# Kernel tuning notes

Hardware: AMD Instinct MI355X
Metric: run time of the kernel (lower is better)

Reference implementation:

```python
import jax, jax.numpy as jnp
import numpy as np

N_NODES = 100000
N_EDGES = 1600000
N_GRAPHS = 64
F = 128  # feature_dim == hidden_dim == embedding_dim
NUM_CONVS = 3


def _layernorm(h, g, b, eps=1e-5):
    mu = jnp.mean(h, axis=-1, keepdims=True)
    var = jnp.var(h, axis=-1, keepdims=True)
    return (h - mu) * jax.lax.rsqrt(var + eps) * g + b


def setup_inputs() -> dict:
    key = jax.random.key(0)
    ks = jax.random.split(key, 12)
    s = 1.0 / np.sqrt(F)
    return {
        "x": jax.random.normal(ks[0], (N_NODES, F), jnp.float32),
        "edge_index": jax.random.randint(ks[1], (2, N_EDGES), 0, N_NODES, jnp.int32),
        "batch_vec": jnp.sort(jax.random.randint(ks[2], (N_NODES,), 0, N_GRAPHS, jnp.int32)),
        "gammas": 1.0 + 0.1 * jax.random.normal(ks[3], (N_GRAPHS, NUM_CONVS), jnp.float32),
        "betas": 0.1 * jax.random.normal(ks[4], (N_GRAPHS, NUM_CONVS), jnp.float32),
        "pre_W0": s * jax.random.normal(ks[5], (F, F), jnp.float32),
        "pre_b0": jnp.zeros((F,), jnp.float32),
        "pre_W1": s * jax.random.normal(ks[6], (F, F), jnp.float32),
        "pre_b1": jnp.zeros((F,), jnp.float32),
        "gin_W": s * jax.random.normal(ks[7], (NUM_CONVS, 2, F, F), jnp.float32),
        "gin_b": jnp.zeros((NUM_CONVS, 2, F), jnp.float32),
        "post_W0": (1.0 / np.sqrt(5 * F)) * jax.random.normal(ks[8], (5 * F, F), jnp.float32),
        "post_b0": jnp.zeros((F,), jnp.float32),
        "post_ln_g": jnp.ones((F,), jnp.float32),
        "post_ln_b": jnp.zeros((F,), jnp.float32),
        "post_W1": s * jax.random.normal(ks[9], (F, F), jnp.float32),
        "post_b1": jnp.zeros((F,), jnp.float32),
    }


def reference(x, edge_index, batch_vec, gammas, betas,
              pre_W0, pre_b0, pre_W1, pre_b1,
              gin_W, gin_b,
              post_W0, post_b0, post_ln_g, post_ln_b, post_W1, post_b1):
    n = x.shape[0]
    src, dst = edge_index[0], edge_index[1]

    # preprocess MLP (2 layers, ReLU between, batch_norm='none')
    h = jnp.dot(jax.nn.relu(jnp.dot(x, pre_W0) + pre_b0), pre_W1) + pre_b1
    jump_xs = [x, h]

    # per-node FiLM coefficients (repeat_interleave over sorted batch == gather)
    g_nodes = gammas[batch_vec]  # [N, num_convs]
    b_nodes = betas[batch_vec]   # [N, num_convs]

    for i in range(NUM_CONVS):
        # GINConv, eps=0: MLP(h_i + sum_{j->i} h_j)
        aggr = jax.ops.segment_sum(h[src], dst, num_segments=n)
        z = h + aggr
        h = jnp.dot(jax.nn.relu(jnp.dot(z, gin_W[i, 0]) + gin_b[i, 0]), gin_W[i, 1]) + gin_b[i, 1]
        # FiLM modulation
        h = h * g_nodes[:, i:i + 1] + b_nodes[:, i:i + 1]
        jump_xs.append(h)

    # jumping knowledge 'cat'
    h = jnp.concatenate(jump_xs, axis=-1)  # [N, feature + 4*hidden]

    # postprocess MLP with LayerNorm (batch_norm='layer'); dropout p=0 (eval)
    z = jnp.dot(h, post_W0) + post_b0
    z = jax.nn.relu(_layernorm(z, post_ln_g, post_ln_b))
    return jnp.dot(z, post_W1) + post_b1
```

## Files before the change

kernel.cpp:

```cpp
#include <hip/hip_runtime.h>
#include <stdint.h>

#define FDIM 128
constexpr int EP_NONE = 0, EP_RELU = 1, EP_FILM = 2, EP_LNRELU = 3;

typedef __attribute__((ext_vector_type(8))) short short8v;
typedef __attribute__((ext_vector_type(4))) float f32x4;
typedef __attribute__((ext_vector_type(4))) unsigned int u32x4;

struct Srcs { const float* p[5]; };
struct WPtrs { const float* p[14]; };

__device__ __forceinline__ short f2bf(float f) {
  unsigned u = __float_as_uint(f);
  u = (u + 0x7fffu + ((u >> 16) & 1u)) >> 16;
  return (short)u;
}
__device__ __forceinline__ float bf2f(short s) {
  return __uint_as_float(((unsigned)(unsigned short)s) << 16);
}


__global__ __launch_bounds__(256)
void k_hist(const int* __restrict__ dst, int* __restrict__ cnt, int E) {
  int e = blockIdx.x * 256 + threadIdx.x;
  if (e < E) atomicAdd(&cnt[dst[e]], 1);
}

__global__ __launch_bounds__(1024)
void k_scan_block(const int* __restrict__ cnt, int* __restrict__ scanned,
                  int* __restrict__ partials, int n) {
  __shared__ int sd[1024];
  int tid = threadIdx.x;
  int i = blockIdx.x * 1024 + tid;
  int v = (i < n) ? cnt[i] : 0;
  sd[tid] = v; __syncthreads();
  for (int off = 1; off < 1024; off <<= 1) {
    int t = (tid >= off) ? sd[tid - off] : 0;
    __syncthreads();
    sd[tid] += t;
    __syncthreads();
  }
  if (i < n) scanned[i] = sd[tid] - v;
  if (tid == 1023) partials[blockIdx.x] = sd[1023];
}

__global__ __launch_bounds__(128)
void k_scan_small(const int* __restrict__ partials, int* __restrict__ p2, int nb) {
  __shared__ int sd[128];
  int tid = threadIdx.x;
  int v = (tid < nb) ? partials[tid] : 0;
  sd[tid] = v; __syncthreads();
  for (int off = 1; off < 128; off <<= 1) {
    int t = (tid >= off) ? sd[tid - off] : 0;
    __syncthreads();
    sd[tid] += t;
    __syncthreads();
  }
  p2[tid] = sd[tid] - v;
}

__global__ __launch_bounds__(256)
void k_finalize(const int* __restrict__ scanned, const int* __restrict__ p2,
                int* __restrict__ indptr, int* __restrict__ cursor, int n, int E) {
  int i = blockIdx.x * 256 + threadIdx.x;
  if (i < n) {
    int v = scanned[i] + p2[i >> 10];
    indptr[i] = v;
    cursor[i] = v;
  }
  if (i == 0) indptr[n] = E;
}

__global__ __launch_bounds__(256)
void k_scatter(const int* __restrict__ src, const int* __restrict__ dst,
               int* __restrict__ cursor, int* __restrict__ eids, int E) {
  int e = blockIdx.x * 256 + threadIdx.x;
  if (e < E) {
    int p = atomicAdd(&cursor[dst[e]], 1);
    eids[p] = src[e];
  }
}


__global__ __launch_bounds__(256)
void k_aggr(const float* __restrict__ h, const int* __restrict__ indptr,
            const int* __restrict__ eids, float* __restrict__ z, int n) {
  int lane = threadIdx.x & 63;
  int node = blockIdx.x * 4 + (threadIdx.x >> 6);
  if (node >= n) return;
  float2 acc = *(const float2*)&h[(size_t)node * FDIM + lane * 2];
  int s = indptr[node], e = indptr[node + 1];
  for (int base = s; base < e; base += 64) {
    int cnt = min(64, e - base);
    int eid = (base + lane < e) ? eids[base + lane] : 0;
    int j = 0;
    for (; j + 8 <= cnt; j += 8) {
      float2 v[8];
      #pragma unroll
      for (int t = 0; t < 8; ++t) {
        int sn = __shfl(eid, j + t, 64);
        v[t] = *(const float2*)&h[(size_t)sn * FDIM + lane * 2];
      }
      #pragma unroll
      for (int t = 0; t < 8; ++t) { acc.x += v[t].x; acc.y += v[t].y; }
    }
    for (; j < cnt; ++j) {
      int sn = __shfl(eid, j, 64);
      float2 hv = *(const float2*)&h[(size_t)sn * FDIM + lane * 2];
      acc.x += hv.x; acc.y += hv.y;
    }
  }
  *(float2*)&z[(size_t)node * FDIM + lane * 2] = acc;
}


__global__ __launch_bounds__(256)
void k_wt(WPtrs wp, short* __restrict__ wtHi, short* __restrict__ wtLo) {
  const int m = blockIdx.x;
  const float* __restrict__ W = wp.p[m];
  const int t = threadIdx.x;
  #pragma unroll
  for (int u = 0; u < 8; ++u) {
    int chunk = t + u * 256;
    int c = chunk >> 4, kc = chunk & 15;
    short8v hi, lo;
    #pragma unroll
    for (int j = 0; j < 8; ++j) {
      float w = W[(kc * 8 + j) * FDIM + c];
      short h = f2bf(w);
      hi[j] = h;
      lo[j] = f2bf(w - bf2f(h));
    }
    int off = m * 16384 + c * FDIM + kc * 8;
    *(short8v*)(wtHi + off) = hi;
    *(short8v*)(wtLo + off) = lo;
  }
}


__device__ __forceinline__ void load_panel(float4 (&P)[2][4][2], const float* __restrict__ A,
                                           int row0, int lr, int lg, int n) {
  const float4 f4z = {0.f, 0.f, 0.f, 0.f};
  #pragma unroll
  for (int s = 0; s < 2; ++s) {
    const int r = row0 + s * 16 + lr;
    const bool ok = r < n;
    const float* Ar = A + (size_t)r * FDIM + lg * 8;
    #pragma unroll
    for (int k = 0; k < 4; ++k) {
      P[s][k][0] = ok ? *(const float4*)(Ar + k * 32) : f4z;
      P[s][k][1] = ok ? *(const float4*)(Ar + k * 32 + 4) : f4z;
    }
  }
}

__device__ __forceinline__ void compute_panel(const float4 (&P)[2][4][2], f32x4 (&acc)[2][8],
                                              const short* __restrict__ wtHi,
                                              const short* __restrict__ wtLo,
                                              int wbase, int lr, int lg) {
  #pragma unroll
  for (int k = 0; k < 4; ++k) {
    short8v ah[2], al[2];
    #pragma unroll
    for (int s = 0; s < 2; ++s) {
      const float vv[8] = {P[s][k][0].x, P[s][k][0].y, P[s][k][0].z, P[s][k][0].w,
                           P[s][k][1].x, P[s][k][1].y, P[s][k][1].z, P[s][k][1].w};
      #pragma unroll
      for (int j = 0; j < 8; ++j) {
        short h = f2bf(vv[j]);
        ah[s][j] = h;
        al[s][j] = f2bf(vv[j] - bf2f(h));
      }
    }
    #pragma unroll
    for (int f = 0; f < 8; ++f) {
      const int boff = wbase + (f * 16 + lr) * FDIM + k * 32 + lg * 8;
      short8v bh = *(const short8v*)(wtHi + boff);
      short8v bl = *(const short8v*)(wtLo + boff);
      acc[0][f] = __builtin_amdgcn_mfma_f32_16x16x32_bf16(ah[0], bh, acc[0][f], 0, 0, 0);
      acc[1][f] = __builtin_amdgcn_mfma_f32_16x16x32_bf16(ah[1], bh, acc[1][f], 0, 0, 0);
      acc[0][f] = __builtin_amdgcn_mfma_f32_16x16x32_bf16(al[0], bh, acc[0][f], 0, 0, 0);
      acc[1][f] = __builtin_amdgcn_mfma_f32_16x16x32_bf16(al[1], bh, acc[1][f], 0, 0, 0);
      acc[0][f] = __builtin_amdgcn_mfma_f32_16x16x32_bf16(ah[0], bl, acc[0][f], 0, 0, 0);
      acc[1][f] = __builtin_amdgcn_mfma_f32_16x16x32_bf16(ah[1], bl, acc[1][f], 0, 0, 0);
    }
  }
}

template<int NSRC, int EPI1, int EPI2>
__global__ __launch_bounds__(256, 2)
void k_mlp(Srcs srcs, const short* __restrict__ wtHi, const short* __restrict__ wtLo,
           int m0, int m1, const float* __restrict__ b1, const float* __restrict__ b2,
           float* __restrict__ out, int n,
           const int* __restrict__ bvec, const float* __restrict__ gam,
           const float* __restrict__ bet, int conv,
           const float* __restrict__ lng, const float* __restrict__ lnb) {
  __shared__ unsigned int lds[128 * FDIM];

  const int tid = threadIdx.x;
  const int lane = tid & 63;
  const int w = tid >> 6;
  const int lr = lane & 15;
  const int lg = lane >> 4;
  const int row0 = blockIdx.x * 128 + w * 32;

  f32x4 acc[2][8];
  #pragma unroll
  for (int s = 0; s < 2; ++s)
    #pragma unroll
    for (int f = 0; f < 8; ++f) acc[s][f] = (f32x4){0.f, 0.f, 0.f, 0.f};

  float4 P0[2][4][2], P1[2][4][2];
  load_panel(P0, srcs.p[0], row0, lr, lg, n);
  if constexpr (NSRC >= 2) load_panel(P1, srcs.p[1], row0, lr, lg, n);
  compute_panel(P0, acc, wtHi, wtLo, (m0 + 0) * 16384, lr, lg);
  if constexpr (NSRC >= 3) load_panel(P0, srcs.p[2], row0, lr, lg, n);
  if constexpr (NSRC >= 2) compute_panel(P1, acc, wtHi, wtLo, (m0 + 1) * 16384, lr, lg);
  if constexpr (NSRC >= 4) load_panel(P1, srcs.p[3], row0, lr, lg, n);
  if constexpr (NSRC >= 3) compute_panel(P0, acc, wtHi, wtLo, (m0 + 2) * 16384, lr, lg);
  if constexpr (NSRC >= 5) load_panel(P0, srcs.p[4], row0, lr, lg, n);
  if constexpr (NSRC >= 4) compute_panel(P1, acc, wtHi, wtLo, (m0 + 3) * 16384, lr, lg);
  if constexpr (NSRC >= 5) compute_panel(P0, acc, wtHi, wtLo, (m0 + 4) * 16384, lr, lg);

  {
    float bb[8];
    #pragma unroll
    for (int f = 0; f < 8; ++f) bb[f] = b1[f * 16 + lr];
    #pragma unroll
    for (int s = 0; s < 2; ++s) {
      #pragma unroll
      for (int f = 0; f < 8; ++f)
        #pragma unroll
        for (int i = 0; i < 4; ++i) acc[s][f][i] += bb[f];

      if constexpr (EPI1 == EP_LNRELU) {
        float sm[4] = {0.f, 0.f, 0.f, 0.f}, sq[4] = {0.f, 0.f, 0.f, 0.f};
        #pragma unroll
        for (int f = 0; f < 8; ++f)
          #pragma unroll
          for (int i = 0; i < 4; ++i) {
            float v = acc[s][f][i];
            sm[i] += v; sq[i] += v * v;
          }
        #pragma unroll
        for (int m = 1; m < 16; m <<= 1)
          #pragma unroll
          for (int i = 0; i < 4; ++i) {
            sm[i] += __shfl_xor(sm[i], m, 64);
            sq[i] += __shfl_xor(sq[i], m, 64);
          }
        float gg[8], bn[8];
        #pragma unroll
        for (int f = 0; f < 8; ++f) { gg[f] = lng[f * 16 + lr]; bn[f] = lnb[f * 16 + lr]; }
        #pragma unroll
        for (int i = 0; i < 4; ++i) {
          const float mu = sm[i] * (1.f / FDIM);
          const float var = sq[i] * (1.f / FDIM) - mu * mu;
          const float rs = rsqrtf(var + 1e-5f);
          #pragma unroll
          for (int f = 0; f < 8; ++f)
            acc[s][f][i] = fmaxf((acc[s][f][i] - mu) * rs * gg[f] + bn[f], 0.f);
        }
      } else {
        #pragma unroll
        for (int f = 0; f < 8; ++f)
          #pragma unroll
          for (int i = 0; i < 4; ++i) acc[s][f][i] = fmaxf(acc[s][f][i], 0.f);
      }

      #pragma unroll
      for (int f = 0; f < 8; ++f)
        #pragma unroll
        for (int i = 0; i < 4; ++i) {
          float v = acc[s][f][i];
          short hi = f2bf(v);
          short lo = f2bf(v - bf2f(hi));
          unsigned pk = (unsigned)(unsigned short)hi | ((unsigned)(unsigned short)lo << 16);
          const int rl = w * 32 + s * 16 + 4 * lg + i;
          const int c = f * 16 + lr;
          lds[rl * FDIM + (c ^ ((rl & 7) * 8))] = pk;
        }
    }
  }
  __syncthreads();

  f32x4 acc2[2][8];
  #pragma unroll
  for (int s = 0; s < 2; ++s)
    #pragma unroll
    for (int f = 0; f < 8; ++f) acc2[s][f] = (f32x4){0.f, 0.f, 0.f, 0.f};

  const int wbase2 = m1 * 16384;
  #pragma unroll
  for (int k = 0; k < 4; ++k) {
    short8v ah[2], al[2];
    #pragma unroll
    for (int s = 0; s < 2; ++s) {
      const int rl = w * 32 + s * 16 + lr;
      const int kidx = k * 32 + lg * 8;
      const int idx = rl * FDIM + (kidx ^ ((rl & 7) * 8));
      u32x4 u0 = *(const u32x4*)&lds[idx];
      u32x4 u1 = *(const u32x4*)&lds[idx + 4];
      #pragma unroll
      for (int j = 0; j < 4; ++j) {
        ah[s][j]     = (short)(u0[j] & 0xffffu);
        al[s][j]     = (short)(u0[j] >> 16);
        ah[s][j + 4] = (short)(u1[j] & 0xffffu);
        al[s][j + 4] = (short)(u1[j] >> 16);
      }
    }
    #pragma unroll
    for (int f = 0; f < 8; ++f) {
      const int boff = wbase2 + (f * 16 + lr) * FDIM + k * 32 + lg * 8;
      short8v bh = *(const short8v*)(wtHi + boff);
      short8v bl = *(const short8v*)(wtLo + boff);
      acc2[0][f] = __builtin_amdgcn_mfma_f32_16x16x32_bf16(ah[0], bh, acc2[0][f], 0, 0, 0);
      acc2[1][f] = __builtin_amdgcn_mfma_f32_16x16x32_bf16(ah[1], bh, acc2[1][f], 0, 0, 0);
      acc2[0][f] = __builtin_amdgcn_mfma_f32_16x16x32_bf16(al[0], bh, acc2[0][f], 0, 0, 0);
      acc2[1][f] = __builtin_amdgcn_mfma_f32_16x16x32_bf16(al[1], bh, acc2[1][f], 0, 0, 0);
      acc2[0][f] = __builtin_amdgcn_mfma_f32_16x16x32_bf16(ah[0], bl, acc2[0][f], 0, 0, 0);
      acc2[1][f] = __builtin_amdgcn_mfma_f32_16x16x32_bf16(ah[1], bl, acc2[1][f], 0, 0, 0);
    }
  }

  {
    float bb[8];
    #pragma unroll
    for (int f = 0; f < 8; ++f) bb[f] = b2[f * 16 + lr];
    #pragma unroll
    for (int s = 0; s < 2; ++s)
      #pragma unroll
      for (int i = 0; i < 4; ++i) {
        const int r = row0 + s * 16 + 4 * lg + i;
        if (r >= n) continue;
        float g = 1.f, be = 0.f;
        if constexpr (EPI2 == EP_FILM) {
          int b = bvec[r];
          g = gam[b * 3 + conv];
          be = bet[b * 3 + conv];
        }
        #pragma unroll
        for (int f = 0; f < 8; ++f) {
          float o = acc2[s][f][i] + bb[f];
          if constexpr (EPI2 == EP_FILM) o = o * g + be;
          out[(size_t)r * FDIM + f * 16 + lr] = o;
        }
      }
  }
}


extern "C" void kernel_launch(void* const* d_in, const int* in_sizes, int n_in,
                              void* d_out, int out_size, void* d_ws, size_t ws_size,
                              hipStream_t stream) {
  const float* x       = (const float*)d_in[0];
  const int*   eidx    = (const int*)d_in[1];
  const int*   bvec    = (const int*)d_in[2];
  const float* gam     = (const float*)d_in[3];
  const float* bet     = (const float*)d_in[4];
  const float* pre_W0  = (const float*)d_in[5];
  const float* pre_b0  = (const float*)d_in[6];
  const float* pre_W1  = (const float*)d_in[7];
  const float* pre_b1  = (const float*)d_in[8];
  const float* gin_W   = (const float*)d_in[9];
  const float* gin_b   = (const float*)d_in[10];
  const float* post_W0 = (const float*)d_in[11];
  const float* post_b0 = (const float*)d_in[12];
  const float* lng     = (const float*)d_in[13];
  const float* lnb     = (const float*)d_in[14];
  const float* post_W1 = (const float*)d_in[15];
  const float* post_b1 = (const float*)d_in[16];

  const int n = in_sizes[0] / FDIM;
  const int E = in_sizes[1] / 2;
  const int* esrc = eidx;
  const int* edst = eidx + E;
  float* out = (float*)d_out;

  const size_t NF = (size_t)n * FDIM;
  float* fws = (float*)d_ws;
  float* h0  = fws;
  float* h1  = fws + NF;
  float* h2  = fws + 2 * NF;
  float* h3  = fws + 3 * NF;
  float* zb  = out;
  int* iws      = (int*)(fws + 4 * NF);
  int* counts   = iws;
  int* scanned  = iws + n;
  int* indptr   = iws + 2 * n;
  int* cursor   = iws + 3 * n + 1;
  int* partials = iws + 4 * n + 1;
  int* p2       = partials + 128;
  int* eids     = p2 + 128;
  uintptr_t wtb = ((uintptr_t)(eids + E) + 15) & ~(uintptr_t)15;
  short* wtHi = (short*)wtb;
  short* wtLo = wtHi + 14 * 16384;

  WPtrs wp;
  wp.p[0] = pre_W0;
  wp.p[1] = pre_W1;
  for (int i = 0; i < 6; ++i) wp.p[2 + i] = gin_W + (size_t)i * 16384;
  for (int j = 0; j < 5; ++j) wp.p[8 + j] = post_W0 + (size_t)j * 16384;
  wp.p[13] = post_W1;
  k_wt<<<14, 256, 0, stream>>>(wp, wtHi, wtLo);

  hipMemsetAsync(counts, 0, (size_t)n * sizeof(int), stream);
  k_hist<<<(E + 255) / 256, 256, 0, stream>>>(edst, counts, E);
  const int nb = (n + 1023) / 1024;
  k_scan_block<<<nb, 1024, 0, stream>>>(counts, scanned, partials, n);
  k_scan_small<<<1, 128, 0, stream>>>(partials, p2, nb);
  k_finalize<<<(n + 255) / 256, 256, 0, stream>>>(scanned, p2, indptr, cursor, n, E);
  k_scatter<<<(E + 255) / 256, 256, 0, stream>>>(esrc, edst, cursor, eids, E);

  const int gb = (n + 127) / 128;

  Srcs sx{{x, nullptr, nullptr, nullptr, nullptr}};
  k_mlp<1, EP_RELU, EP_NONE><<<gb, 256, 0, stream>>>(
      sx, wtHi, wtLo, 0, 1, pre_b0, pre_b1, h0, n,
      nullptr, nullptr, nullptr, 0, nullptr, nullptr);

  float* hprev = h0;
  float* houts[3] = {h1, h2, h3};
  for (int i = 0; i < 3; ++i) {
    k_aggr<<<(n + 3) / 4, 256, 0, stream>>>(hprev, indptr, eids, zb, n);
    Srcs sz{{zb, nullptr, nullptr, nullptr, nullptr}};
    k_mlp<1, EP_RELU, EP_FILM><<<gb, 256, 0, stream>>>(
        sz, wtHi, wtLo, 2 + 2 * i, 3 + 2 * i,
        gin_b + (size_t)(2 * i) * FDIM, gin_b + (size_t)(2 * i + 1) * FDIM,
        houts[i], n, bvec, gam, bet, i, nullptr, nullptr);
    hprev = houts[i];
  }

  Srcs sj{{x, h0, h1, h2, h3}};
  k_mlp<5, EP_LNRELU, EP_NONE><<<gb, 256, 0, stream>>>(
      sj, wtHi, wtLo, 8, 13, post_b0, post_b1, out, n,
      nullptr, nullptr, nullptr, 0, lng, lnb);
}
```

Before: 1.412 ms.

## Stage MLP input panels via async global-to-LDS loads and shrink block tile

The MLP kernel now stages input row panels into double-buffered LDS with global_load_lds and explicit vmcnt waits, so loading the next source panel overlaps the MFMA work on the current one. Each wave now handles 16 rows instead of 32, so a block covers 64 rows and twice as many blocks launch. The intermediate hidden tile stays in per-wave LDS, which removes the block-wide barrier. The aggregation loop is also unrolled to 16 with clamped indices in place of a scalar tail loop. Halving rows per wave means each weight fragment load feeds fewer MFMAs, which raises weight traffic per row.

```diff
diff --git a/kernel.cpp b/kernel.cpp
--- a/kernel.cpp
+++ b/kernel.cpp
@@ -19,6 +19,17 @@
 __device__ __forceinline__ float bf2f(short s) {
   return __uint_as_float(((unsigned)(unsigned short)s) << 16);
 }
+
+__device__ __forceinline__ void gload16(const float* g, float* l) {
+  __builtin_amdgcn_global_load_lds(
+      (const __attribute__((address_space(1))) void*)g,
+      (__attribute__((address_space(3))) void*)l, 16, 0, 0);
+}
+
+#define VM_WAIT8 do { asm volatile("s_waitcnt vmcnt(8)" ::: "memory"); \
+                      __builtin_amdgcn_sched_barrier(0); } while (0)
+#define VM_WAIT0 do { asm volatile("s_waitcnt vmcnt(0)" ::: "memory"); \
+                      __builtin_amdgcn_sched_barrier(0); } while (0)
 
 
 __global__ __launch_bounds__(256)
@@ -94,21 +105,17 @@
   for (int base = s; base < e; base += 64) {
     int cnt = min(64, e - base);
     int eid = (base + lane < e) ? eids[base + lane] : 0;
-    int j = 0;
-    for (; j + 8 <= cnt; j += 8) {
-      float2 v[8];
-      #pragma unroll
-      for (int t = 0; t < 8; ++t) {
-        int sn = __shfl(eid, j + t, 64);
+    for (int j = 0; j < cnt; j += 16) {
+      float2 v[16];
+      #pragma unroll
+      for (int t = 0; t < 16; ++t) {
+        int idx = j + t;
+        int sn = __shfl(eid, idx < cnt ? idx : cnt - 1, 64);
         v[t] = *(const float2*)&h[(size_t)sn * FDIM + lane * 2];
       }
       #pragma unroll
-      for (int t = 0; t < 8; ++t) { acc.x += v[t].x; acc.y += v[t].y; }
-    }
-    for (; j < cnt; ++j) {
-      int sn = __shfl(eid, j, 64);
-      float2 hv = *(const float2*)&h[(size_t)sn * FDIM + lane * 2];
-      acc.x += hv.x; acc.y += hv.y;
+      for (int t = 0; t < 16; ++t)
+        if (j + t < cnt) { acc.x += v[t].x; acc.y += v[t].y; }
     }
   }
   *(float2*)&z[(size_t)node * FDIM + lane * 2] = acc;
@@ -139,55 +146,6 @@
 }
 
 
-__device__ __forceinline__ void load_panel(float4 (&P)[2][4][2], const float* __restrict__ A,
-                                           int row0, int lr, int lg, int n) {
-  const float4 f4z = {0.f, 0.f, 0.f, 0.f};
-  #pragma unroll
-  for (int s = 0; s < 2; ++s) {
-    const int r = row0 + s * 16 + lr;
-    const bool ok = r < n;
-    const float* Ar = A + (size_t)r * FDIM + lg * 8;
-    #pragma unroll
-    for (int k = 0; k < 4; ++k) {
-      P[s][k][0] = ok ? *(const float4*)(Ar + k * 32) : f4z;
-      P[s][k][1] = ok ? *(const float4*)(Ar + k * 32 + 4) : f4z;
-    }
-  }
-}
-
-__device__ __forceinline__ void compute_panel(const float4 (&P)[2][4][2], f32x4 (&acc)[2][8],
-                                              const short* __restrict__ wtHi,
-                                              const short* __restrict__ wtLo,
-                                              int wbase, int lr, int lg) {
-  #pragma unroll
-  for (int k = 0; k < 4; ++k) {
-    short8v ah[2], al[2];
-    #pragma unroll
-    for (int s = 0; s < 2; ++s) {
-      const float vv[8] = {P[s][k][0].x, P[s][k][0].y, P[s][k][0].z, P[s][k][0].w,
-                           P[s][k][1].x, P[s][k][1].y, P[s][k][1].z, P[s][k][1].w};
-      #pragma unroll
-      for (int j = 0; j < 8; ++j) {
-        short h = f2bf(vv[j]);
-        ah[s][j] = h;
-        al[s][j] = f2bf(vv[j] - bf2f(h));
-      }
-    }
-    #pragma unroll
-    for (int f = 0; f < 8; ++f) {
-      const int boff = wbase + (f * 16 + lr) * FDIM + k * 32 + lg * 8;
-      short8v bh = *(const short8v*)(wtHi + boff);
-      short8v bl = *(const short8v*)(wtLo + boff);
-      acc[0][f] = __builtin_amdgcn_mfma_f32_16x16x32_bf16(ah[0], bh, acc[0][f], 0, 0, 0);
-      acc[1][f] = __builtin_amdgcn_mfma_f32_16x16x32_bf16(ah[1], bh, acc[1][f], 0, 0, 0);
-      acc[0][f] = __builtin_amdgcn_mfma_f32_16x16x32_bf16(al[0], bh, acc[0][f], 0, 0, 0);
-      acc[1][f] = __builtin_amdgcn_mfma_f32_16x16x32_bf16(al[1], bh, acc[1][f], 0, 0, 0);
-      acc[0][f] = __builtin_amdgcn_mfma_f32_16x16x32_bf16(ah[0], bl, acc[0][f], 0, 0, 0);
-      acc[1][f] = __builtin_amdgcn_mfma_f32_16x16x32_bf16(ah[1], bl, acc[1][f], 0, 0, 0);
-    }
-  }
-}
-
 template<int NSRC, int EPI1, int EPI2>
 __global__ __launch_bounds__(256, 2)
 void k_mlp(Srcs srcs, const short* __restrict__ wtHi, const short* __restrict__ wtLo,
@@ -196,131 +154,156 @@
            const int* __restrict__ bvec, const float* __restrict__ gam,
            const float* __restrict__ bet, int conv,
            const float* __restrict__ lng, const float* __restrict__ lnb) {
-  __shared__ unsigned int lds[128 * FDIM];
+  __shared__ float lds[2][4][16][FDIM];
 
   const int tid = threadIdx.x;
   const int lane = tid & 63;
   const int w = tid >> 6;
   const int lr = lane & 15;
   const int lg = lane >> 4;
-  const int row0 = blockIdx.x * 128 + w * 32;
-
-  f32x4 acc[2][8];
+  const int row0w = blockIdx.x * 64 + w * 16;
+
+  float* Lb0 = &lds[0][w][0][0];
+  float* Lb1 = &lds[1][w][0][0];
+
+  auto STAGE = [&](const float* __restrict__ A, float* Lw) {
+    const int rl2 = lane >> 5;
+    const int g = lane & 31;
+    #pragma unroll
+    for (int t = 0; t < 8; ++t) {
+      const int rl = t * 2 + rl2;
+      const int grow = min(row0w + rl, n - 1);
+      const int gs = g ^ (rl & 7);
+      gload16(A + (size_t)grow * FDIM + gs * 4, Lw + t * 256);
+    }
+  };
+
+  auto COMPUTE = [&](const float* Lw, int wbase, f32x4 (&acc)[8]) {
+    #pragma unroll
+    for (int k = 0; k < 4; ++k) {
+      const int ga = k * 8 + lg * 2;
+      const float4 a0 = *(const float4*)&Lw[lr * FDIM + ((ga ^ (lr & 7)) << 2)];
+      const float4 a1 = *(const float4*)&Lw[lr * FDIM + (((ga + 1) ^ (lr & 7)) << 2)];
+      const float vv[8] = {a0.x, a0.y, a0.z, a0.w, a1.x, a1.y, a1.z, a1.w};
+      short8v ah, al;
+      #pragma unroll
+      for (int j = 0; j < 8; ++j) {
+        short h = f2bf(vv[j]);
+        ah[j] = h;
+        al[j] = f2bf(vv[j] - bf2f(h));
+      }
+      #pragma unroll
+      for (int f = 0; f < 8; ++f) {
+        const int boff = wbase + (f * 16 + lr) * FDIM + k * 32 + lg * 8;
+        short8v bh = *(const short8v*)(wtHi + boff);
+        short8v bl = *(const short8v*)(wtLo + boff);
+        acc[f] = __builtin_amdgcn_mfma_f32_16x16x32_bf16(ah, bh, acc[f], 0, 0, 0);
+        acc[f] = __builtin_amdgcn_mfma_f32_16x16x32_bf16(al, bh, acc[f], 0, 0, 0);
+        acc[f] = __builtin_amdgcn_mfma_f32_16x16x32_bf16(ah, bl, acc[f], 0, 0, 0);
+      }
+    }
+  };
+
+  f32x4 acc[8];
   #pragma unroll
-  for (int s = 0; s < 2; ++s)
-    #pragma unroll
-    for (int f = 0; f < 8; ++f) acc[s][f] = (f32x4){0.f, 0.f, 0.f, 0.f};
-
-  float4 P0[2][4][2], P1[2][4][2];
-  load_panel(P0, srcs.p[0], row0, lr, lg, n);
-  if constexpr (NSRC >= 2) load_panel(P1, srcs.p[1], row0, lr, lg, n);
-  compute_panel(P0, acc, wtHi, wtLo, (m0 + 0) * 16384, lr, lg);
-  if constexpr (NSRC >= 3) load_panel(P0, srcs.p[2], row0, lr, lg, n);
-  if constexpr (NSRC >= 2) compute_panel(P1, acc, wtHi, wtLo, (m0 + 1) * 16384, lr, lg);
-  if constexpr (NSRC >= 4) load_panel(P1, srcs.p[3], row0, lr, lg, n);
-  if constexpr (NSRC >= 3) compute_panel(P0, acc, wtHi, wtLo, (m0 + 2) * 16384, lr, lg);
-  if constexpr (NSRC >= 5) load_panel(P0, srcs.p[4], row0, lr, lg, n);
-  if constexpr (NSRC >= 4) compute_panel(P1, acc, wtHi, wtLo, (m0 + 3) * 16384, lr, lg);
-  if constexpr (NSRC >= 5) compute_panel(P0, acc, wtHi, wtLo, (m0 + 4) * 16384, lr, lg);
-
+  for (int f = 0; f < 8; ++f) acc[f] = (f32x4){0.f, 0.f, 0.f, 0.f};
+
+  STAGE(srcs.p[0], Lb0);
+  if constexpr (NSRC >= 2) STAGE(srcs.p[1], Lb1);
+
+  #pragma unroll
+  for (int js = 0; js < NSRC; ++js) {
+    if (js < NSRC - 1) { VM_WAIT8; } else { VM_WAIT0; }
+    COMPUTE((js & 1) ? Lb1 : Lb0, (m0 + js) * 16384, acc);
+    __builtin_amdgcn_sched_barrier(0);
+    if (js + 2 < NSRC) STAGE(srcs.p[js + 2], (js & 1) ? Lb1 : Lb0);
+  }
+
+  unsigned int* Ib = (unsigned int*)((NSRC & 1) ? Lb1 : Lb0);
   {
     float bb[8];
     #pragma unroll
     for (int f = 0; f < 8; ++f) bb[f] = b1[f * 16 + lr];
     #pragma unroll
-    for (int s = 0; s < 2; ++s) {
-      #pragma unroll
-      for (int f = 0; f < 8; ++f)
-        #pragma unroll
-        for (int i = 0; i < 4; ++i) acc[s][f][i] += bb[f];
-
-      if constexpr (EPI1 == EP_LNRELU) {
-        float sm[4] = {0.f, 0.f, 0.f, 0.f}, sq[4] = {0.f, 0.f, 0.f, 0.f};
-        #pragma unroll
-        for (int f = 0; f < 8; ++f)
-          #pragma unroll
-          for (int i = 0; i < 4; ++i) {
-            float v = acc[s][f][i];
-            sm[i] += v; sq[i] += v * v;
-          }
-        #pragma unroll
-        for (int m = 1; m < 16; m <<= 1)
-          #pragma unroll
-          for (int i = 0; i < 4; ++i) {
-            sm[i] += __shfl_xor(sm[i], m, 64);
-            sq[i] += __shfl_xor(sq[i], m, 64);
-          }
-        float gg[8], bn[8];
-        #pragma unroll
-        for (int f = 0; f < 8; ++f) { gg[f] = lng[f * 16 + lr]; bn[f] = lnb[f * 16 + lr]; }
-        #pragma unroll
-        for (int i = 0; i < 4; ++i) {
-          const float mu = sm[i] * (1.f / FDIM);
-          const float var = sq[i] * (1.f / FDIM) - mu * mu;
-          const float rs = rsqrtf(var + 1e-5f);
-          #pragma unroll
-          for (int f = 0; f < 8; ++f)
-            acc[s][f][i] = fmaxf((acc[s][f][i] - mu) * rs * gg[f] + bn[f], 0.f);
-        }
-      } else {
-        #pragma unroll
-        for (int f = 0; f < 8; ++f)
-          #pragma unroll
-          for (int i = 0; i < 4; ++i) acc[s][f][i] = fmaxf(acc[s][f][i], 0.f);
-      }
-
+    for (int f = 0; f < 8; ++f)
+      #pragma unroll
+      for (int i = 0; i < 4; ++i) acc[f][i] += bb[f];
+
+    if constexpr (EPI1 == EP_LNRELU) {
+      float sm[4] = {0.f, 0.f, 0.f, 0.f}, sq[4] = {0.f, 0.f, 0.f, 0.f};
       #pragma unroll
       for (int f = 0; f < 8; ++f)
         #pragma unroll
         for (int i = 0; i < 4; ++i) {
-          float v = acc[s][f][i];
-          short hi = f2bf(v);
-          short lo = f2bf(v - bf2f(hi));
-          unsigned pk = (unsigned)(unsigned short)hi | ((unsigned)(unsigned short)lo << 16);
-          const int rl = w * 32 + s * 16 + 4 * lg + i;
-          const int c = f * 16 + lr;
-          lds[rl * FDIM + (c ^ ((rl & 7) * 8))] = pk;
+          float v = acc[f][i];
+          sm[i] += v; sq[i] += v * v;
         }
-    }
-  }
-  __syncthreads();
-
-  f32x4 acc2[2][8];
+      #pragma unroll
+      for (int m = 1; m < 16; m <<= 1)
+        #pragma unroll
+        for (int i = 0; i < 4; ++i) {
+          sm[i] += __shfl_xor(sm[i], m, 64);
+          sq[i] += __shfl_xor(sq[i], m, 64);
+        }
+      float gg[8], bn[8];
+      #pragma unroll
+      for (int f = 0; f < 8; ++f) { gg[f] = lng[f * 16 + lr]; bn[f] = lnb[f * 16 + lr]; }
+      #pragma unroll
+      for (int i = 0; i < 4; ++i) {
+        const float mu = sm[i] * (1.f / FDIM);
+        const float var = sq[i] * (1.f / FDIM) - mu * mu;
+        const float rs = rsqrtf(var + 1e-5f);
+        #pragma unroll
+        for (int f = 0; f < 8; ++f)
+          acc[f][i] = fmaxf((acc[f][i] - mu) * rs * gg[f] + bn[f], 0.f);
+      }
+    } else {
+      #pragma unroll
+      for (int f = 0; f < 8; ++f)
+        #pragma unroll
+        for (int i = 0; i < 4; ++i) acc[f][i] = fmaxf(acc[f][i], 0.f);
+    }
+
+    #pragma unroll
+    for (int f = 0; f < 8; ++f)
+      #pragma unroll
+      for (int i = 0; i < 4; ++i) {
+        float v = acc[f][i];
+        short hi = f2bf(v);
+        short lo = f2bf(v - bf2f(hi));
+        unsigned pk = (unsigned)(unsigned short)hi | ((unsigned)(unsigned short)lo << 16);
+        const int r = 4 * lg + i;
+        const int c = f * 16 + lr;
+        Ib[r * FDIM + ((((c >> 2) ^ (r & 7)) << 2) | (c & 3))] = pk;
+      }
+  }
+
+  f32x4 acc2[8];
   #pragma unroll
-  for (int s = 0; s < 2; ++s)
-    #pragma unroll
-    for (int f = 0; f < 8; ++f) acc2[s][f] = (f32x4){0.f, 0.f, 0.f, 0.f};
+  for (int f = 0; f < 8; ++f) acc2[f] = (f32x4){0.f, 0.f, 0.f, 0.f};
 
   const int wbase2 = m1 * 16384;
   #pragma unroll
   for (int k = 0; k < 4; ++k) {
-    short8v ah[2], al[2];
-    #pragma unroll
-    for (int s = 0; s < 2; ++s) {
-      const int rl = w * 32 + s * 16 + lr;
-      const int kidx = k * 32 + lg * 8;
-      const int idx = rl * FDIM + (kidx ^ ((rl & 7) * 8));
-      u32x4 u0 = *(const u32x4*)&lds[idx];
-      u32x4 u1 = *(const u32x4*)&lds[idx + 4];
-      #pragma unroll
-      for (int j = 0; j < 4; ++j) {
-        ah[s][j]     = (short)(u0[j] & 0xffffu);
-        al[s][j]     = (short)(u0[j] >> 16);
-        ah[s][j + 4] = (short)(u1[j] & 0xffffu);
-        al[s][j + 4] = (short)(u1[j] >> 16);
-      }
+    const int ga = k * 8 + lg * 2;
+    u32x4 u0 = *(const u32x4*)&Ib[lr * FDIM + ((ga ^ (lr & 7)) << 2)];
+    u32x4 u1 = *(const u32x4*)&Ib[lr * FDIM + (((ga + 1) ^ (lr & 7)) << 2)];
+    short8v ah, al;
+    #pragma unroll
+    for (int j = 0; j < 4; ++j) {
+      ah[j]     = (short)(u0[j] & 0xffffu);
+      al[j]     = (short)(u0[j] >> 16);
+      ah[j + 4] = (short)(u1[j] & 0xffffu);
+      al[j + 4] = (short)(u1[j] >> 16);
     }
     #pragma unroll
     for (int f = 0; f < 8; ++f) {
       const int boff = wbase2 + (f * 16 + lr) * FDIM + k * 32 + lg * 8;
       short8v bh = *(const short8v*)(wtHi + boff);
       short8v bl = *(const short8v*)(wtLo + boff);
-      acc2[0][f] = __builtin_amdgcn_mfma_f32_16x16x32_bf16(ah[0], bh, acc2[0][f], 0, 0, 0);
-      acc2[1][f] = __builtin_amdgcn_mfma_f32_16x16x32_bf16(ah[1], bh, acc2[1][f], 0, 0, 0);
-      acc2[0][f] = __builtin_amdgcn_mfma_f32_16x16x32_bf16(al[0], bh, acc2[0][f], 0, 0, 0);
-      acc2[1][f] = __builtin_amdgcn_mfma_f32_16x16x32_bf16(al[1], bh, acc2[1][f], 0, 0, 0);
-      acc2[0][f] = __builtin_amdgcn_mfma_f32_16x16x32_bf16(ah[0], bl, acc2[0][f], 0, 0, 0);
-      acc2[1][f] = __builtin_amdgcn_mfma_f32_16x16x32_bf16(ah[1], bl, acc2[1][f], 0, 0, 0);
+      acc2[f] = __builtin_amdgcn_mfma_f32_16x16x32_bf16(ah, bh, acc2[f], 0, 0, 0);
+      acc2[f] = __builtin_amdgcn_mfma_f32_16x16x32_bf16(al, bh, acc2[f], 0, 0, 0);
+      acc2[f] = __builtin_amdgcn_mfma_f32_16x16x32_bf16(ah, bl, acc2[f], 0, 0, 0);
     }
   }
 
@@ -329,24 +312,23 @@
     #pragma unroll
     for (int f = 0; f < 8; ++f) bb[f] = b2[f * 16 + lr];
     #pragma unroll
-    for (int s = 0; s < 2; ++s)
-      #pragma unroll
-      for (int i = 0; i < 4; ++i) {
-        const int r = row0 + s * 16 + 4 * lg + i;
-        if (r >= n) continue;
-        float g = 1.f, be = 0.f;
-        if constexpr (EPI2 == EP_FILM) {
-          int b = bvec[r];
-          g = gam[b * 3 + conv];
-          be = bet[b * 3 + conv];
-        }
-        #pragma unroll
-        for (int f = 0; f < 8; ++f) {
-          float o = acc2[s][f][i] + bb[f];
-          if constexpr (EPI2 == EP_FILM) o = o * g + be;
-          out[(size_t)r * FDIM + f * 16 + lr] = o;
-        }
-      }
+    for (int i = 0; i < 4; ++i) {
+      const int r = row0w + 4 * lg + i;
+      if (r >= n) continue;
+      float g = 1.f, be = 0.f;
+      if constexpr (EPI2 == EP_FILM) {
+        int b = bvec[r];
+        g = gam[b * 3 + conv];
+        be = bet[b * 3 + conv];
+      }
+      #pragma unroll
+      for (int f = 0; f < 8; ++f) {
+        float o = acc2[f][i] + bb[f];
+        if constexpr (EPI2 == EP_RELU) o = fmaxf(o, 0.f);
+        if constexpr (EPI2 == EP_FILM) o = o * g + be;
+        out[(size_t)r * FDIM + f * 16 + lr] = o;
+      }
+    }
   }
 }
 
@@ -413,7 +395,7 @@
   k_finalize<<<(n + 255) / 256, 256, 0, stream>>>(scanned, p2, indptr, cursor, n, E);
   k_scatter<<<(E + 255) / 256, 256, 0, stream>>>(esrc, edst, cursor, eids, E);
 
-  const int gb = (n + 127) / 128;
+  const int gb = (n + 63) / 64;
 
   Srcs sx{{x, nullptr, nullptr, nullptr, nullptr}};
   k_mlp<1, EP_RELU, EP_NONE><<<gb, 256, 0, stream>>>(
```

New measurement: 1.546 ms. 1.1x slower.
